# Performance work log

Hardware: AMD Instinct MI355X
Metric: run time of the kernel (lower is better)

## Reference

```python
import jax, jax.numpy as jnp
import numpy as np

B, S1, S2, D, H, FFN = 4, 1024, 1024, 1024, 16, 4096
DK = D // H  # 64
EPS = 1e-5


def layer_norm(x, g, b):
    m = jnp.mean(x, axis=-1, keepdims=True)
    v = jnp.mean((x - m) ** 2, axis=-1, keepdims=True)
    return (x - m) * jax.lax.rsqrt(v + EPS) * g + b


def cross_attention(y, kvn, mask, qw, kw, vw, ow, ob):
    # y: [B,S1,D], kvn: [B,S2,D], mask: [B,S2] int (0 -> masked)
    q = (y @ qw).reshape(B, S1, H, DK)
    k = (kvn @ kw).reshape(B, S2, H, DK)
    v = (kvn @ vw).reshape(B, S2, H, DK)
    attn = jnp.einsum('bqhd,bkhd->bhqk', q, k) / np.sqrt(DK).astype(np.float32)
    attn = jnp.where(mask[:, None, None, :] == 0, jnp.float32(-1e9), attn)
    attn = jax.nn.softmax(attn, axis=-1)
    out = jnp.einsum('bhqk,bkhd->bqhd', attn, v).reshape(B, S1, H * DK)
    return out @ ow + ob


def setup_inputs() -> dict:
    key = jax.random.key(0)
    ks = jax.random.split(key, 16)
    s = 1.0 / np.sqrt(D)
    inp = {
        'x': jax.random.normal(ks[0], (B, S1, D), jnp.float32),
        'kv': jax.random.normal(ks[1], (B, S2, D), jnp.float32),
        'attn_bias': jax.random.randint(ks[2], (B, S2), 0, 2, jnp.int32),
        'ln1_g': jnp.ones((D,), jnp.float32),
        'ln1_b': jnp.zeros((D,), jnp.float32),
        'qw0': jax.random.normal(ks[3], (D, D), jnp.float32) * s,
        'kw0': jax.random.normal(ks[4], (D, D), jnp.float32) * s,
        'vw0': jax.random.normal(ks[5], (D, D), jnp.float32) * s,
        'ow0': jax.random.normal(ks[6], (D, D), jnp.float32) * s,
        'ob0': jnp.zeros((D,), jnp.float32),
        'qw1': jax.random.normal(ks[7], (D, D), jnp.float32) * s,
        'kw1': jax.random.normal(ks[8], (D, D), jnp.float32) * s,
        'vw1': jax.random.normal(ks[9], (D, D), jnp.float32) * s,
        'ow1': jax.random.normal(ks[10], (D, D), jnp.float32) * s,
        'ob1': jnp.zeros((D,), jnp.float32),
        'ln2_g': jnp.ones((D,), jnp.float32),
        'ln2_b': jnp.zeros((D,), jnp.float32),
        'w1': jax.random.normal(ks[11], (D, FFN), jnp.float32) * s,
        'b1': jnp.zeros((FFN,), jnp.float32),
        'w2': jax.random.normal(ks[12], (FFN, D), jnp.float32) * (1.0 / np.sqrt(FFN)),
        'b2': jnp.zeros((D,), jnp.float32),
    }
    return inp


def reference(x, kv, attn_bias, ln1_g, ln1_b, qw0, kw0, vw0, ow0, ob0,
              qw1, kw1, vw1, ow1, ob1, ln2_g, ln2_b, w1, b1, w2, b2):
    y = layer_norm(x, ln1_g, ln1_b)
    kvn = layer_norm(kv, ln1_g, ln1_b)  # same norm module applied to both
    y = cross_attention(y, kvn, attn_bias, qw0, kw0, vw0, ow0, ob0) + y
    y = cross_attention(y, kvn, attn_bias, qw1, kw1, vw1, ow1, ob1) + y
    x = x + y  # dropout rate 0 -> identity
    y = layer_norm(x, ln2_g, ln2_b)
    y = jax.nn.relu(y @ w1 + b1) @ w2 + b2
    x = x + y
    return x
```

## Files before the change

kernel.cpp:

```cpp
#include <hip/hip_runtime.h>
#include <stdint.h>

typedef unsigned short u16;
typedef __bf16 bf16x8 __attribute__((ext_vector_type(8)));
typedef float f32x4 __attribute__((ext_vector_type(4)));

#define LOG2E 1.4426950408889634f

__device__ __forceinline__ float bf2f(u16 a) {
  union { unsigned u; float f; } v; v.u = ((unsigned)a) << 16; return v.f;
}
__device__ __forceinline__ u16 f2bf(float f) {
  union { float f; unsigned u; } v; v.f = f;
  unsigned r = v.u + 0x7fffu + ((v.u >> 16) & 1u);
  return (u16)(r >> 16);
}
__device__ __forceinline__ u16 f2bf_fast(float f) {
  __bf16 h = (__bf16)f;
  union { __bf16 h; u16 u; } v; v.h = h; return v.u;
}
__device__ __forceinline__ void gl_lds16(const void* g, void* l) {
  __builtin_amdgcn_global_load_lds(
      (const __attribute__((address_space(1))) uint32_t*)g,
      (__attribute__((address_space(3))) uint32_t*)l,
      16, 0, 0);
}

__device__ __forceinline__ int swz(int row, int colu16) {
  return row * 64 + (colu16 ^ (((row ^ (row >> 2)) & 7) << 3));
}

template <int BM, int BN, int MODE>
__global__ __launch_bounds__(256) void gemm_bt(
    const u16* __restrict__ A, const u16* __restrict__ Bt,
    u16* Cbf, float* C32,
    const float* __restrict__ bias,
    const u16* resbf, const float* __restrict__ resx,
    int M, int N, int K)
{
  constexpr int MT = BM / 32, NT = BN / 32;
  constexpr int GA = BM / 32, GB = BN / 32;
  __shared__ u16 sA[BM * 64];
  __shared__ u16 sB[BN * 64];
  const int tid  = threadIdx.x;
  const int wave = tid >> 6, lane = tid & 63;
  const int quad = lane >> 4, l16 = lane & 15;
  const int wm = wave >> 1, wn = wave & 1;
  const int m0 = blockIdx.y * BM, n0 = blockIdx.x * BN;

  f32x4 acc[MT][NT] = {};

  for (int k0 = 0; k0 < K; k0 += 64) {
    __syncthreads();
#pragma unroll
    for (int i = 0; i < GA; ++i) {
      int cb = i * 256 + wave * 64;
      int c = cb + lane;
      int row = c >> 3, kc = c & 7;
      gl_lds16(A + (size_t)(m0 + row) * K + k0 + kc * 8, &sA[cb * 8]);
    }
#pragma unroll
    for (int i = 0; i < GB; ++i) {
      int cb = i * 256 + wave * 64;
      int c = cb + lane;
      int row = c >> 3, kc = c & 7;
      gl_lds16(Bt + (size_t)(n0 + row) * K + k0 + kc * 8, &sB[cb * 8]);
    }
    __syncthreads();

#pragma unroll
    for (int kk = 0; kk < 2; ++kk) {
      bf16x8 fa[MT], fb[NT];
#pragma unroll
      for (int mt = 0; mt < MT; ++mt)
        fa[mt] = *(const bf16x8*)&sA[(wm * (BM / 2) + mt * 16 + l16) * 64 + kk * 32 + quad * 8];
#pragma unroll
      for (int nt = 0; nt < NT; ++nt)
        fb[nt] = *(const bf16x8*)&sB[(wn * (BN / 2) + nt * 16 + l16) * 64 + kk * 32 + quad * 8];
#pragma unroll
      for (int mt = 0; mt < MT; ++mt)
#pragma unroll
        for (int nt = 0; nt < NT; ++nt)
          acc[mt][nt] = __builtin_amdgcn_mfma_f32_16x16x32_bf16(
              fa[mt], fb[nt], acc[mt][nt], 0, 0, 0);
    }
  }

#pragma unroll
  for (int mt = 0; mt < MT; ++mt) {
#pragma unroll
    for (int nt = 0; nt < NT; ++nt) {
#pragma unroll
      for (int r = 0; r < 4; ++r) {
        int row = m0 + wm * (BM / 2) + mt * 16 + quad * 4 + r;
        int col = n0 + wn * (BN / 2) + nt * 16 + l16;
        size_t idx = (size_t)row * N + col;
        float v = acc[mt][nt][r];
        if constexpr (MODE == 0) {
          Cbf[idx] = f2bf(v);
        } else if constexpr (MODE == 1) {
          v += bias[col] + bf2f(resbf[idx]);
          Cbf[idx] = f2bf(v);
        } else if constexpr (MODE == 2) {
          v = fmaxf(v + bias[col], 0.f);
          Cbf[idx] = f2bf(v);
        } else if constexpr (MODE == 3) {
          v += bias[col] + resx[idx] + bf2f(resbf[idx]);
          C32[idx] = v;
        } else {
          C32[idx] = C32[idx] + v;
        }
      }
    }
  }
}

__global__ __launch_bounds__(256) void transpose64(
    const float* __restrict__ in, u16* __restrict__ out, int R, int Cstride)
{
  __shared__ u16 tile[64][72];
  const int r0 = blockIdx.y * 64, c0 = blockIdx.x * 64;
  const int t = threadIdx.x;
  {
    const int lr = t >> 4, lc = (t & 15) * 4;
#pragma unroll
    for (int h = 0; h < 4; ++h) {
      int row = h * 16 + lr;
      float4 vd = *(const float4*)&in[(size_t)(r0 + row) * Cstride + c0 + lc];
      ushort4 ov;
      ov.x = f2bf(vd.x); ov.y = f2bf(vd.y); ov.z = f2bf(vd.z); ov.w = f2bf(vd.w);
      *(ushort4*)&tile[row][lc] = ov;
    }
  }
  __syncthreads();
  {
    const int lr = t >> 3, lv = t & 7;
#pragma unroll
    for (int h = 0; h < 2; ++h) {
      int orow = h * 32 + lr;
      u16 tmp[8];
#pragma unroll
      for (int j = 0; j < 8; ++j) tmp[j] = tile[lv * 8 + j][orow];
      *(uint4*)&out[(size_t)(c0 + orow) * R + r0 + lv * 8] = *(uint4*)tmp;
    }
  }
}

__global__ __launch_bounds__(256) void mask_scan(
    const int* __restrict__ mask, int* __restrict__ sidx, int* __restrict__ nv)
{
  const int b = blockIdx.x, t = threadIdx.x;
  const int wave = t >> 6, lane = t & 63;
  int m[4]; int cnt = 0;
#pragma unroll
  for (int k = 0; k < 4; ++k) { m[k] = (mask[b * 1024 + t * 4 + k] != 0); cnt += m[k]; }
  int sc = cnt;
  for (int sh = 1; sh < 64; sh <<= 1) {
    int u = __shfl_up(sc, sh);
    if (lane >= sh) sc += u;
  }
  __shared__ int wsum[4];
  if (lane == 63) wsum[wave] = sc;
  __syncthreads();
  int woff = 0;
  for (int w = 0; w < wave; ++w) woff += wsum[w];
  int pos = woff + sc - cnt;
#pragma unroll
  for (int k = 0; k < 4; ++k)
    if (m[k]) sidx[b * 1024 + pos++] = t * 4 + k;
  if (t == 255) nv[b] = wsum[0] + wsum[1] + wsum[2] + wsum[3];
}

__global__ __launch_bounds__(256) void vtc_kernel(
    const u16* __restrict__ in, const int* __restrict__ sidx,
    const int* __restrict__ nv, u16* __restrict__ out)
{
  __shared__ u16 tile[64][72];
  const int st = blockIdx.x, bh = blockIdx.y;
  const int b = bh >> 4, h = bh & 15;
  const int t = threadIdx.x;
  const int lr = t >> 3, lv = t & 7;
  const int n = nv[b];
  const u16* srcb = in + (size_t)b * 1024 * 2048 + 1024 + h * 64;
#pragma unroll
  for (int half = 0; half < 2; ++half) {
    int i = st * 64 + half * 32 + lr;
    int s = sidx[b * 1024 + (i < n ? i : n - 1)];
    uint4 vd = *(const uint4*)&srcb[(size_t)s * 2048 + lv * 8];
    *(uint4*)&tile[half * 32 + lr][lv * 8] = vd;
  }
  __syncthreads();
  u16* dst = out + (size_t)bh * 64 * 1024 + st * 64;
#pragma unroll
  for (int half = 0; half < 2; ++half) {
    int orow = half * 32 + lr;
    u16 tmp[8];
#pragma unroll
    for (int j = 0; j < 8; ++j) tmp[j] = tile[lv * 8 + j][orow];
    *(uint4*)&dst[(size_t)orow * 1024 + lv * 8] = *(uint4*)tmp;
  }
}

__global__ __launch_bounds__(256) void ln_kernel(
    const float* __restrict__ x, const float* __restrict__ g,
    const float* __restrict__ b, u16* __restrict__ outbf)
{
  const int row = blockIdx.x, t = threadIdx.x;
  const int wave = t >> 6, lane = t & 63;
  float4 xv = *(const float4*)&x[(size_t)row * 1024 + t * 4];
  float v0 = xv.x, v1 = xv.y, v2 = xv.z, v3 = xv.w;
  float s = v0 + v1 + v2 + v3;
  float s2 = v0 * v0 + v1 * v1 + v2 * v2 + v3 * v3;
  for (int m = 1; m < 64; m <<= 1) { s += __shfl_xor(s, m); s2 += __shfl_xor(s2, m); }
  __shared__ float ps[4], pq[4];
  if (lane == 0) { ps[wave] = s; pq[wave] = s2; }
  __syncthreads();
  s = ps[0] + ps[1] + ps[2] + ps[3];
  s2 = pq[0] + pq[1] + pq[2] + pq[3];
  float mean = s * (1.f / 1024.f);
  float var = s2 * (1.f / 1024.f) - mean * mean;
  float rs = rsqrtf(var + 1e-5f);
  float4 gv = *(const float4*)&g[t * 4];
  float4 bv = *(const float4*)&b[t * 4];
  ushort4 ov;
  ov.x = f2bf((v0 - mean) * rs * gv.x + bv.x);
  ov.y = f2bf((v1 - mean) * rs * gv.y + bv.y);
  ov.z = f2bf((v2 - mean) * rs * gv.z + bv.z);
  ov.w = f2bf((v3 - mean) * rs * gv.w + bv.w);
  *(ushort4*)&outbf[(size_t)row * 1024 + t * 4] = ov;
}

__global__ __launch_bounds__(256) void ln_add_kernel(
    const float* __restrict__ x, const u16* __restrict__ ybf,
    const float* __restrict__ g, const float* __restrict__ b,
    u16* __restrict__ hbf)
{
  const int row = blockIdx.x, t = threadIdx.x;
  const int wave = t >> 6, lane = t & 63;
  float4 xv = *(const float4*)&x[(size_t)row * 1024 + t * 4];
  ushort4 yv = *(const ushort4*)&ybf[(size_t)row * 1024 + t * 4];
  float v0 = xv.x + bf2f(yv.x), v1 = xv.y + bf2f(yv.y);
  float v2 = xv.z + bf2f(yv.z), v3 = xv.w + bf2f(yv.w);
  float s = v0 + v1 + v2 + v3;
  float s2 = v0 * v0 + v1 * v1 + v2 * v2 + v3 * v3;
  for (int m = 1; m < 64; m <<= 1) { s += __shfl_xor(s, m); s2 += __shfl_xor(s2, m); }
  __shared__ float ps[4], pq[4];
  if (lane == 0) { ps[wave] = s; pq[wave] = s2; }
  __syncthreads();
  s = ps[0] + ps[1] + ps[2] + ps[3];
  s2 = pq[0] + pq[1] + pq[2] + pq[3];
  float mean = s * (1.f / 1024.f);
  float var = s2 * (1.f / 1024.f) - mean * mean;
  float rs = rsqrtf(var + 1e-5f);
  float4 gv = *(const float4*)&g[t * 4];
  float4 bv = *(const float4*)&b[t * 4];
  ushort4 ov;
  ov.x = f2bf((v0 - mean) * rs * gv.x + bv.x);
  ov.y = f2bf((v1 - mean) * rs * gv.y + bv.y);
  ov.z = f2bf((v2 - mean) * rs * gv.z + bv.z);
  ov.w = f2bf((v3 - mean) * rs * gv.w + bv.w);
  *(ushort4*)&hbf[(size_t)row * 1024 + t * 4] = ov;
}

__global__ __launch_bounds__(256) void attn_kernel(
    const u16* __restrict__ Q,
    const u16* __restrict__ K,
    const u16* __restrict__ Vt,
    const int* __restrict__ sidx,
    const int* __restrict__ nvp,
    u16* __restrict__ O)
{
  __shared__ u16 sK[64 * 64], sVt[64 * 64], sP[128 * 64];
  const int h = blockIdx.x, qt = blockIdx.y, b = blockIdx.z;
  const int t = threadIdx.x;
  const int wave = t >> 6, lane = t & 63;
  const int quad = lane >> 4, l16 = lane & 15;
  const u16* Qb = Q + (size_t)b * 1024 * 1024 + (size_t)qt * 128 * 1024 + h * 64;
  const u16* Kb = K + (size_t)b * 1024 * 2048 + h * 64;
  const u16* Vb = Vt + (size_t)(b * 16 + h) * 64 * 1024;
  const int n = nvp[b];
  const int jmax = (n + 63) >> 6;
  const int* sb = sidx + b * 1024;

#pragma unroll
  for (int i = 0; i < 4; ++i) {
    int cb = i * 256 + wave * 64;
    int c = cb + lane;
    int row = c >> 3;
    int scc = (c & 7) ^ ((row ^ (row >> 2)) & 7);
    gl_lds16(Qb + (size_t)row * 1024 + scc * 8, &sP[cb * 8]);
  }
  __syncthreads();
  bf16x8 aq[2][2];
#pragma unroll
  for (int g = 0; g < 2; ++g)
#pragma unroll
    for (int ks = 0; ks < 2; ++ks)
      aq[g][ks] = *(const bf16x8*)&sP[swz(wave * 32 + g * 16 + l16, ks * 32 + quad * 8)];

  float m2_[2][4], l_[2][4];
  f32x4 accO[2][4] = {};
#pragma unroll
  for (int g = 0; g < 2; ++g)
#pragma unroll
    for (int r = 0; r < 4; ++r) { m2_[g][r] = -1e30f; l_[g][r] = 0.f; }

  constexpr float QS = 0.125f * LOG2E;

  for (int j = 0; j < jmax; ++j) {
    __syncthreads();
#pragma unroll
    for (int i = 0; i < 2; ++i) {
      int cb = i * 256 + wave * 64;
      int c = cb + lane;
      int row = c >> 3;
      int scc = (c & 7) ^ ((row ^ (row >> 2)) & 7);
      int gi = j * 64 + row;
      int s = sb[gi < n ? gi : n - 1];
      gl_lds16(Kb + (size_t)s * 2048 + scc * 8, &sK[cb * 8]);
      gl_lds16(Vb + (size_t)row * 1024 + j * 64 + scc * 8, &sVt[cb * 8]);
    }
    __syncthreads();

    float mf[4];
#pragma unroll
    for (int nt = 0; nt < 4; ++nt)
      mf[nt] = (j * 64 + nt * 16 + l16 < n) ? 0.f : -1e9f;

#pragma unroll
    for (int g = 0; g < 2; ++g) {
      f32x4 accS[4] = {};
#pragma unroll
      for (int ks = 0; ks < 2; ++ks) {
#pragma unroll
        for (int nt = 0; nt < 4; ++nt) {
          bf16x8 bk = *(const bf16x8*)&sK[swz(nt * 16 + l16, ks * 32 + quad * 8)];
          accS[nt] = __builtin_amdgcn_mfma_f32_16x16x32_bf16(aq[g][ks], bk, accS[nt], 0, 0, 0);
        }
      }
      float vv[4][4], cm_[4];
      bool need = false;
#pragma unroll
      for (int r = 0; r < 4; ++r) {
#pragma unroll
        for (int nt = 0; nt < 4; ++nt) vv[r][nt] = fmaf(accS[nt][r], QS, mf[nt]);
        float cm = fmaxf(fmaxf(vv[r][0], vv[r][1]), fmaxf(vv[r][2], vv[r][3]));
        for (int sh = 1; sh < 16; sh <<= 1) cm = fmaxf(cm, __shfl_xor(cm, sh));
        cm_[r] = cm;
        need = need || (cm > m2_[g][r] + 8.f);
      }
      if (__any(need)) {
#pragma unroll
        for (int r = 0; r < 4; ++r) {
          float nm = fmaxf(m2_[g][r], cm_[r]);
          float al = exp2f(m2_[g][r] - nm);
          m2_[g][r] = nm;
          l_[g][r] *= al;
#pragma unroll
          for (int n2 = 0; n2 < 4; ++n2) accO[g][n2][r] *= al;
        }
      }
#pragma unroll
      for (int r = 0; r < 4; ++r) {
        int prow = wave * 32 + g * 16 + quad * 4 + r;
        float rs = 0.f;
#pragma unroll
        for (int nt = 0; nt < 4; ++nt) {
          float p = exp2f(vv[r][nt] - m2_[g][r]);
          rs += p;
          sP[swz(prow, nt * 16 + l16)] = f2bf_fast(p);
        }
        l_[g][r] += rs;
      }
    }
#pragma unroll
    for (int ks = 0; ks < 2; ++ks) {
      bf16x8 bv[4];
#pragma unroll
      for (int n2 = 0; n2 < 4; ++n2)
        bv[n2] = *(const bf16x8*)&sVt[swz(n2 * 16 + l16, ks * 32 + quad * 8)];
#pragma unroll
      for (int g = 0; g < 2; ++g) {
        bf16x8 ap = *(const bf16x8*)&sP[swz(wave * 32 + g * 16 + l16, ks * 32 + quad * 8)];
#pragma unroll
        for (int n2 = 0; n2 < 4; ++n2)
          accO[g][n2] = __builtin_amdgcn_mfma_f32_16x16x32_bf16(ap, bv[n2], accO[g][n2], 0, 0, 0);
      }
    }
  }

  u16* Ob = O + (size_t)b * 1024 * 1024 + (size_t)qt * 128 * 1024 + h * 64;
#pragma unroll
  for (int g = 0; g < 2; ++g) {
#pragma unroll
    for (int r = 0; r < 4; ++r) {
      float lr = l_[g][r];
      for (int sh = 1; sh < 16; sh <<= 1) lr += __shfl_xor(lr, sh);
      float inv = 1.f / lr;
      int row = wave * 32 + g * 16 + quad * 4 + r;
#pragma unroll
      for (int n2 = 0; n2 < 4; ++n2)
        Ob[(size_t)row * 1024 + n2 * 16 + l16] = f2bf_fast(accO[g][n2][r] * inv);
    }
  }
}

extern "C" void kernel_launch(void* const* d_in, const int* in_sizes, int n_in,
                              void* d_out, int out_size, void* d_ws, size_t ws_size,
                              hipStream_t stream)
{
  const float* x   = (const float*)d_in[0];
  const float* kv  = (const float*)d_in[1];
  const int* attn_bias = (const int*)d_in[2];
  const float* ln1_g = (const float*)d_in[3];
  const float* ln1_b = (const float*)d_in[4];
  const float* qw0 = (const float*)d_in[5];
  const float* kw0 = (const float*)d_in[6];
  const float* vw0 = (const float*)d_in[7];
  const float* ow0 = (const float*)d_in[8];
  const float* ob0 = (const float*)d_in[9];
  const float* qw1 = (const float*)d_in[10];
  const float* kw1 = (const float*)d_in[11];
  const float* vw1 = (const float*)d_in[12];
  const float* ow1 = (const float*)d_in[13];
  const float* ob1 = (const float*)d_in[14];
  const float* ln2_g = (const float*)d_in[15];
  const float* ln2_b = (const float*)d_in[16];
  const float* w1 = (const float*)d_in[17];
  const float* b1 = (const float*)d_in[18];
  const float* w2 = (const float*)d_in[19];
  const float* b2 = (const float*)d_in[20];

  char* ws = (char*)d_ws;
  const size_t MB = 1u << 20;
  u16* Wkv   = (u16*)(ws + 0 * MB);
  u16* Wsm   = (u16*)(ws + 4 * MB);
  int* sidx  = (int*)(ws + 6 * MB);
  int* nvp   = sidx + 4096;
  u16* wtA   = (u16*)(ws + 0 * MB);
  u16* wtB   = (u16*)(ws + 4 * MB);
  u16* ybf   = (u16*)(ws + 8 * MB);
  u16* kvnbf = (u16*)(ws + 16 * MB);
  u16* qbuf  = (u16*)(ws + 24 * MB);
  u16* kvbuf = (u16*)(ws + 32 * MB);
  u16* hbf   = kvnbf;
  u16* fbuf  = kvbuf;
  u16* attnb = (u16*)d_out;
  u16* vT    = (u16*)((char*)d_out + 8 * MB);
  float* out32 = (float*)d_out;

  const dim3 B256(256);
  const dim3 gT(16, 16);
  const dim3 gGemmN1k(8, 64);
  const dim3 gGemm2k(16, 64);
  const dim3 gVt(16, 64);
  const dim3 gAttn(16, 8, 4);

  mask_scan<<<4, B256, 0, stream>>>(attn_bias, sidx, nvp);

  ln_kernel<<<4096, B256, 0, stream>>>(x,  ln1_g, ln1_b, ybf);
  ln_kernel<<<4096, B256, 0, stream>>>(kv, ln1_g, ln1_b, kvnbf);

  for (int layer = 0; layer < 2; ++layer) {
    const float* qw = layer ? qw1 : qw0;
    const float* kw = layer ? kw1 : kw0;
    const float* vw = layer ? vw1 : vw0;
    const float* ow = layer ? ow1 : ow0;
    const float* ob = layer ? ob1 : ob0;

    transpose64<<<gT, B256, 0, stream>>>(kw, Wkv, 1024, 1024);
    transpose64<<<gT, B256, 0, stream>>>(vw, Wkv + 1024 * 1024, 1024, 1024);
    gemm_bt<64, 128, 0><<<gGemm2k, B256, 0, stream>>>(
        kvnbf, Wkv, kvbuf, nullptr, nullptr, nullptr, nullptr, 4096, 2048, 1024);
    transpose64<<<gT, B256, 0, stream>>>(qw, Wsm, 1024, 1024);
    gemm_bt<64, 128, 0><<<gGemmN1k, B256, 0, stream>>>(
        ybf, Wsm, qbuf, nullptr, nullptr, nullptr, nullptr, 4096, 1024, 1024);
    vtc_kernel<<<gVt, B256, 0, stream>>>(kvbuf, sidx, nvp, vT);

    attn_kernel<<<gAttn, B256, 0, stream>>>(qbuf, kvbuf, vT, sidx, nvp, attnb);

    transpose64<<<gT, B256, 0, stream>>>(ow, Wsm, 1024, 1024);
    gemm_bt<64, 128, 1><<<gGemmN1k, B256, 0, stream>>>(
        attnb, Wsm, ybf, nullptr, ob, ybf, nullptr, 4096, 1024, 1024);
  }

  ln_add_kernel<<<4096, B256, 0, stream>>>(x, ybf, ln2_g, ln2_b, hbf);

  for (int band = 0; band < 2; ++band) {
    transpose64<<<dim3(32, 16), B256, 0, stream>>>(w1 + band * 2048, wtA, 1024, 4096);
    transpose64<<<dim3(16, 32), B256, 0, stream>>>(w2 + (size_t)band * 2048 * 1024,
                                                   wtB, 2048, 1024);
    gemm_bt<64, 128, 2><<<gGemm2k, B256, 0, stream>>>(
        hbf, wtA, fbuf, nullptr, b1 + band * 2048, nullptr, nullptr,
        4096, 2048, 1024);
    if (band == 0) {
      gemm_bt<64, 128, 3><<<gGemmN1k, B256, 0, stream>>>(
          fbuf, wtB, nullptr, out32, b2, ybf, x, 4096, 1024, 2048);
    } else {
      gemm_bt<64, 128, 4><<<gGemmN1k, B256, 0, stream>>>(
          fbuf, wtB, nullptr, out32, nullptr, nullptr, nullptr, 4096, 1024, 2048);
    }
  }
}
```

Measured before the change: 584.6 us.

## Compact unmasked KV rows before projection and skip masked-row GEMM tiles

```diff
diff --git a/kernel.cpp b/kernel.cpp
--- a/kernel.cpp
+++ b/kernel.cpp
@@ -36,7 +36,7 @@
     u16* Cbf, float* C32,
     const float* __restrict__ bias,
     const u16* resbf, const float* __restrict__ resx,
-    int M, int N, int K)
+    int M, int N, int K, const int* __restrict__ rowcnt)
 {
   constexpr int MT = BM / 32, NT = BN / 32;
   constexpr int GA = BM / 32, GB = BN / 32;
@@ -46,7 +46,14 @@
   const int wave = tid >> 6, lane = tid & 63;
   const int quad = lane >> 4, l16 = lane & 15;
   const int wm = wave >> 1, wn = wave & 1;
-  const int m0 = blockIdx.y * BM, n0 = blockIdx.x * BN;
+  const int nwg = gridDim.x * gridDim.y;
+  const int bid = blockIdx.y * gridDim.x + blockIdx.x;
+  const int sw  = (bid & 7) * (nwg >> 3) + (bid >> 3);
+  const int m0 = (sw / gridDim.x) * BM, n0 = (sw % gridDim.x) * BN;
+  if (rowcnt) {
+    int lim = (rowcnt[m0 >> 10] + 63) & ~63;
+    if ((m0 & 1023) >= lim) return;
+  }
 
   f32x4 acc[MT][NT] = {};
 
@@ -171,9 +178,24 @@
   if (t == 255) nv[b] = wsum[0] + wsum[1] + wsum[2] + wsum[3];
 }
 
+__global__ __launch_bounds__(256) void gather_kv(
+    const u16* __restrict__ src, const int* __restrict__ sidx,
+    const int* __restrict__ nv, u16* __restrict__ dst)
+{
+  const int t = threadIdx.x, wave = t >> 6, lane = t & 63;
+  const int row = blockIdx.x * 4 + wave;
+  const int b = row >> 10, i = row & 1023;
+  const int n = nv[b];
+  const int s = sidx[b * 1024 + (i < n ? i : n - 1)];
+  const uint4* sp = (const uint4*)&src[((size_t)(b << 10) + s) * 1024];
+  uint4* dp = (uint4*)&dst[(size_t)row * 1024];
+  dp[lane] = sp[lane];
+  dp[lane + 64] = sp[lane + 64];
+}
+
 __global__ __launch_bounds__(256) void vtc_kernel(
-    const u16* __restrict__ in, const int* __restrict__ sidx,
-    const int* __restrict__ nv, u16* __restrict__ out)
+    const u16* __restrict__ in, const int* __restrict__ nv,
+    u16* __restrict__ out)
 {
   __shared__ u16 tile[64][72];
   const int st = blockIdx.x, bh = blockIdx.y;
@@ -185,7 +207,7 @@
 #pragma unroll
   for (int half = 0; half < 2; ++half) {
     int i = st * 64 + half * 32 + lr;
-    int s = sidx[b * 1024 + (i < n ? i : n - 1)];
+    int s = i < n ? i : n - 1;
     uint4 vd = *(const uint4*)&srcb[(size_t)s * 2048 + lv * 8];
     *(uint4*)&tile[half * 32 + lr][lv * 8] = vd;
   }
@@ -266,7 +288,6 @@
     const u16* __restrict__ Q,
     const u16* __restrict__ K,
     const u16* __restrict__ Vt,
-    const int* __restrict__ sidx,
     const int* __restrict__ nvp,
     u16* __restrict__ O)
 {
@@ -280,7 +301,6 @@
   const u16* Vb = Vt + (size_t)(b * 16 + h) * 64 * 1024;
   const int n = nvp[b];
   const int jmax = (n + 63) >> 6;
-  const int* sb = sidx + b * 1024;
 
 #pragma unroll
   for (int i = 0; i < 4; ++i) {
@@ -315,9 +335,7 @@
       int c = cb + lane;
       int row = c >> 3;
       int scc = (c & 7) ^ ((row ^ (row >> 2)) & 7);
-      int gi = j * 64 + row;
-      int s = sb[gi < n ? gi : n - 1];
-      gl_lds16(Kb + (size_t)s * 2048 + scc * 8, &sK[cb * 8]);
+      gl_lds16(Kb + (size_t)(j * 64 + row) * 2048 + scc * 8, &sK[cb * 8]);
       gl_lds16(Vb + (size_t)row * 1024 + j * 64 + scc * 8, &sVt[cb * 8]);
     }
     __syncthreads();
@@ -440,10 +458,10 @@
   u16* wtA   = (u16*)(ws + 0 * MB);
   u16* wtB   = (u16*)(ws + 4 * MB);
   u16* ybf   = (u16*)(ws + 8 * MB);
-  u16* kvnbf = (u16*)(ws + 16 * MB);
+  u16* kvc   = (u16*)(ws + 16 * MB);
   u16* qbuf  = (u16*)(ws + 24 * MB);
   u16* kvbuf = (u16*)(ws + 32 * MB);
-  u16* hbf   = kvnbf;
+  u16* hbf   = kvc;
   u16* fbuf  = kvbuf;
   u16* attnb = (u16*)d_out;
   u16* vT    = (u16*)((char*)d_out + 8 * MB);
@@ -459,7 +477,8 @@
   mask_scan<<<4, B256, 0, stream>>>(attn_bias, sidx, nvp);
 
   ln_kernel<<<4096, B256, 0, stream>>>(x,  ln1_g, ln1_b, ybf);
-  ln_kernel<<<4096, B256, 0, stream>>>(kv, ln1_g, ln1_b, kvnbf);
+  ln_kernel<<<4096, B256, 0, stream>>>(kv, ln1_g, ln1_b, qbuf);
+  gather_kv<<<1024, B256, 0, stream>>>(qbuf, sidx, nvp, kvc);
 
   for (int layer = 0; layer < 2; ++layer) {
     const float* qw = layer ? qw1 : qw0;
@@ -471,17 +490,20 @@
     transpose64<<<gT, B256, 0, stream>>>(kw, Wkv, 1024, 1024);
     transpose64<<<gT, B256, 0, stream>>>(vw, Wkv + 1024 * 1024, 1024, 1024);
     gemm_bt<64, 128, 0><<<gGemm2k, B256, 0, stream>>>(
-        kvnbf, Wkv, kvbuf, nullptr, nullptr, nullptr, nullptr, 4096, 2048, 1024);
+        kvc, Wkv, kvbuf, nullptr, nullptr, nullptr, nullptr,
+        4096, 2048, 1024, nvp);
     transpose64<<<gT, B256, 0, stream>>>(qw, Wsm, 1024, 1024);
     gemm_bt<64, 128, 0><<<gGemmN1k, B256, 0, stream>>>(
-        ybf, Wsm, qbuf, nullptr, nullptr, nullptr, nullptr, 4096, 1024, 1024);
-    vtc_kernel<<<gVt, B256, 0, stream>>>(kvbuf, sidx, nvp, vT);
-
-    attn_kernel<<<gAttn, B256, 0, stream>>>(qbuf, kvbuf, vT, sidx, nvp, attnb);
+        ybf, Wsm, qbuf, nullptr, nullptr, nullptr, nullptr,
+        4096, 1024, 1024, nullptr);
+    vtc_kernel<<<gVt, B256, 0, stream>>>(kvbuf, nvp, vT);
+
+    attn_kernel<<<gAttn, B256, 0, stream>>>(qbuf, kvbuf, vT, nvp, attnb);
 
     transpose64<<<gT, B256, 0, stream>>>(ow, Wsm, 1024, 1024);
     gemm_bt<64, 128, 1><<<gGemmN1k, B256, 0, stream>>>(
-        attnb, Wsm, ybf, nullptr, ob, ybf, nullptr, 4096, 1024, 1024);
+        attnb, Wsm, ybf, nullptr, ob, ybf, nullptr,
+        4096, 1024, 1024, nullptr);
   }
 
   ln_add_kernel<<<4096, B256, 0, stream>>>(x, ybf, ln2_g, ln2_b, hbf);
@@ -492,13 +514,14 @@
                                                    wtB, 2048, 1024);
     gemm_bt<64, 128, 2><<<gGemm2k, B256, 0, stream>>>(
         hbf, wtA, fbuf, nullptr, b1 + band * 2048, nullptr, nullptr,
-        4096, 2048, 1024);
+        4096, 2048, 1024, nullptr);
     if (band == 0) {
       gemm_bt<64, 128, 3><<<gGemmN1k, B256, 0, stream>>>(
-          fbuf, wtB, nullptr, out32, b2, ybf, x, 4096, 1024, 2048);
+          fbuf, wtB, nullptr, out32, b2, ybf, x, 4096, 1024, 2048, nullptr);
     } else {
       gemm_bt<64, 128, 4><<<gGemmN1k, B256, 0, stream>>>(
-          fbuf, wtB, nullptr, out32, nullptr, nullptr, nullptr, 4096, 1024, 2048);
-    }
-  }
-}
+          fbuf, wtB, nullptr, out32, nullptr, nullptr, nullptr,
+          4096, 1024, 2048, nullptr);
+    }
+  }
+}
```

After: 585.1 us. About the same (+0.1%).
